# Performance work log

Measured on AMD Instinct MI355X. Metric: run time of the kernel, lower is better.

Reference implementation:

```python
import jax, jax.numpy as jnp
import numpy as np

BETA = 1e-7

def pearson_corr(x, y):
    # torch.std is Bessel-corrected (ddof=1); corr clamped to [-1,1]
    n = x.shape[-1]
    cx = x - jnp.mean(x, axis=-1, keepdims=True)
    cy = y - jnp.mean(y, axis=-1, keepdims=True)
    cov = jnp.sum(cx * cy, axis=-1, keepdims=True) / (n - 1)
    xs = jnp.std(x, axis=-1, keepdims=True, ddof=1)
    ys = jnp.std(y, axis=-1, keepdims=True, ddof=1)
    return jnp.clip(cov / (xs * ys + BETA), -1.0, 1.0)

def pearson_loss(p, t):
    return jnp.mean(1.0 - pearson_corr(p, t))

def self_cos_sim(x):
    # x: [B,T,C] -> cosine-similarity map [B,T,T]
    num = jnp.einsum('btc,bsc->bts', x, x)
    d = jnp.sqrt(jnp.sum(x * x, axis=-1, keepdims=True))  # [B,T,1]
    den = d @ jnp.swapaxes(d, 1, 2)                        # [B,T,T]
    return num / den

def turn_into_waves(ssm):
    # Assumed Turn_map_into_waves: average SSM rows -> [B,T]
    return jnp.mean(ssm, axis=1)

def psd(x):
    # Assumed FFT_Batch: power spectrum along last dim
    return jnp.abs(jnp.fft.rfft(x, axis=-1)) ** 2

def loss_distill_pyramid(on_ssm, tg_ssm):
    w_on = turn_into_waves(on_ssm)
    w_tg = turn_into_waves(tg_ssm)
    mse = jnp.mean((on_ssm - tg_ssm) ** 2) + jnp.mean((w_on - w_tg) ** 2)
    return mse + pearson_loss(on_ssm, tg_ssm) + pearson_loss(w_on, w_tg)

def loss_reg(ssm):
    # Vectorized replacement of per-diagonal nested loops + torch.std.
    # For offset k in [1, n-2]: std over the k-th superdiagonal (m = n-k
    # elements, Bessel-corrected), scaled by m/20; mean over offsets & batch.
    n = ssm.shape[-1]
    ii, jj = np.triu_indices(n, k=1)
    seg = jj - ii - 1                               # segment = offset-1 in [0, n-2]
    onehot = jax.nn.one_hot(jnp.asarray(seg), n - 1, dtype=ssm.dtype)  # [M, n-1]
    vals = ssm[:, ii, jj]                           # [B, M] upper-tri gather
    s1 = vals @ onehot                              # per-diagonal sums   [B, n-1]
    s2 = (vals * vals) @ onehot                     # per-diagonal sum-sq [B, n-1]
    m = jnp.asarray(n - 1 - np.arange(n - 1), dtype=ssm.dtype)
    var = jnp.where(m > 1, (s2 - s1 * s1 / m) / jnp.maximum(m - 1, 1.0), 0.0)
    std = jnp.sqrt(jnp.maximum(var, 0.0)) * m / 20.0
    return jnp.mean(std[:, : n - 2])                # original drops last diagonal

def loss_freq(ssm):
    waves = turn_into_waves(ssm)
    p = psd(waves)
    L = p.shape[-1]
    lf, hf = int(0.5 * L / 30.0), int(3 * L / 30.0)
    p = p[:, : L // 2]
    p = p / jnp.max(p, axis=-1, keepdims=True)
    return jnp.mean(jnp.sum(p, axis=-1) / jnp.sum(p[:, lf:hf], axis=-1) - 1.0)

def loss_distill_rppg(on, tg):
    temporal = pearson_loss(on, tg)
    L = on.shape[-1]
    lf, hf, vhf = int(0.5 * L / 30.0), int(3 * L / 30.0), int(15 * L / 30.0)
    so = psd(on)[:, :vhf]
    st = psd(tg)[:, :vhf]
    so = so / jnp.max(so, axis=-1, keepdims=True)
    st = st / jnp.max(st, axis=-1, keepdims=True)
    partition = jnp.sum(so, axis=-1) / jnp.sum(so[:, lf:hf], axis=-1) - 1.0
    return temporal + pearson_loss(so, st) + jnp.mean(partition)

def setup_inputs() -> dict:
    key = jax.random.key(0)
    k1, k2, k3, k4 = jax.random.split(key, 4)
    B, T, C, L = 128, 256, 768, 576
    return {
        'pyr_online': jax.random.normal(k1, (B, T, C), dtype=jnp.float32),
        'pyr_target': jax.random.normal(k2, (B, T, C), dtype=jnp.float32),
        'rppg_online': jax.random.normal(k3, (B, L), dtype=jnp.float32),
        'rppg_target': jax.random.normal(k4, (B, L), dtype=jnp.float32),
    }

def reference(pyr_online, pyr_target, rppg_online, rppg_target):
    tg_ssm = self_cos_sim(jax.lax.stop_gradient(pyr_target))
    on_ssm = self_cos_sim(pyr_online)
    loss_pyramid = loss_distill_pyramid(on_ssm, tg_ssm) * 0.5
    loss_r = loss_reg(on_ssm) * 0.5          # single pyramid level (len=1)
    loss_f = loss_freq(on_ssm) * 0.2
    loss_rppg = loss_distill_rppg(rppg_online, jax.lax.stop_gradient(rppg_target)) * 0.5
    total = loss_rppg + loss_pyramid + loss_r + loss_f
    return (total, loss_pyramid, loss_rppg, loss_r, loss_f)
```

## Files before the change

### kernel.cpp

```cpp
#include <hip/hip_runtime.h>
#include <hip/hip_bf16.h>

#define NB 128
#define NT 256
#define NC 768
#define NL 576

constexpr size_t OFF_P1    = 4096;
constexpr size_t OFF_WON   = 135168;
constexpr size_t OFF_WTG   = 167936;
constexpr size_t OFF_PW    = 200704;
constexpr size_t OFF_FRQ   = 200960;
constexpr size_t OFF_FREQR = 209152;
constexpr size_t OFF_RG    = 209280;
constexpr size_t OFF_RPG   = 241920;
constexpr size_t OFF_SO    = 242304;
constexpr size_t OFF_ST    = 279168;
constexpr size_t OFF_SSM_ON_B = (size_t)2 * 1024 * 1024;
constexpr size_t OFF_SSM_TG_B = OFF_SSM_ON_B + (size_t)NB * NT * NT * 2;

typedef __attribute__((ext_vector_type(8))) short short8v;
typedef __attribute__((ext_vector_type(4))) float f32x4;

__device__ __forceinline__ unsigned short f2bf(float f) {
    __hip_bfloat16 h = __float2bfloat16(f);
    unsigned short u; __builtin_memcpy(&u, &h, 2); return u;
}
__device__ __forceinline__ float bf2f(unsigned short u) {
    __hip_bfloat16 h; __builtin_memcpy(&h, &u, 2); return __bfloat162float(h);
}

__device__ __forceinline__ float sin2pi(float x) {
    x -= floorf(x + 0.5f);
    float x2 = x * x;
    float p = 3.8199526f;
    p = p * x2 - 15.094643f;
    p = p * x2 + 42.058693f;
    p = p * x2 - 76.705860f;
    p = p * x2 + 81.605249f;
    p = p * x2 - 41.341702f;
    p = p * x2 + 6.2831853f;
    return p * x;
}
__device__ __forceinline__ float cos2pi(float x) { return sin2pi(x + 0.25f); }

__device__ __forceinline__ float blockSum(float v, float* tmp) {
    int lane = threadIdx.x & 63, wid = threadIdx.x >> 6;
#pragma unroll
    for (int o = 32; o; o >>= 1) v += __shfl_down(v, o, 64);
    __syncthreads();
    if (lane == 0) tmp[wid] = v;
    __syncthreads();
    return tmp[0] + tmp[1] + tmp[2] + tmp[3];
}
__device__ __forceinline__ float blockMax(float v, float* tmp) {
    int lane = threadIdx.x & 63, wid = threadIdx.x >> 6;
#pragma unroll
    for (int o = 32; o; o >>= 1) v = fmaxf(v, __shfl_down(v, o, 64));
    __syncthreads();
    if (lane == 0) tmp[wid] = v;
    __syncthreads();
    return fmaxf(fmaxf(tmp[0], tmp[1]), fmaxf(tmp[2], tmp[3]));
}
__device__ __forceinline__ float pearson1m(float S0, float S1, float S2, float S3,
                                           float S4, float n) {
    float cov = (S4 - S0 * S1 / n) / (n - 1.f);
    float xs = sqrtf(fmaxf((S2 - S0 * S0 / n) / (n - 1.f), 0.f));
    float ys = sqrtf(fmaxf((S3 - S1 * S1 / n) / (n - 1.f), 0.f));
    float corr = fminf(1.f, fmaxf(-1.f, cov / (xs * ys + 1e-7f)));
    return 1.f - corr;
}

__device__ __forceinline__ float stage32(unsigned short* dstrow, const float* p, int sw) {
    float sq = 0.f;
#pragma unroll
    for (int half = 0; half < 2; half++) {
        float4 a = *reinterpret_cast<const float4*>(p + 16 * half);
        float4 b = *reinterpret_cast<const float4*>(p + 16 * half + 4);
        float4 c = *reinterpret_cast<const float4*>(p + 16 * half + 8);
        float4 d = *reinterpret_cast<const float4*>(p + 16 * half + 12);
        sq += a.x * a.x + a.y * a.y + a.z * a.z + a.w * a.w;
        sq += b.x * b.x + b.y * b.y + b.z * b.z + b.w * b.w;
        sq += c.x * c.x + c.y * c.y + c.z * c.z + c.w * c.w;
        sq += d.x * d.x + d.y * d.y + d.z * d.z + d.w * d.w;
        short8v v0, v1;
        v0[0] = (short)f2bf(a.x); v0[1] = (short)f2bf(a.y);
        v0[2] = (short)f2bf(a.z); v0[3] = (short)f2bf(a.w);
        v0[4] = (short)f2bf(b.x); v0[5] = (short)f2bf(b.y);
        v0[6] = (short)f2bf(b.z); v0[7] = (short)f2bf(b.w);
        v1[0] = (short)f2bf(c.x); v1[1] = (short)f2bf(c.y);
        v1[2] = (short)f2bf(c.z); v1[3] = (short)f2bf(c.w);
        v1[4] = (short)f2bf(d.x); v1[5] = (short)f2bf(d.y);
        v1[6] = (short)f2bf(d.z); v1[7] = (short)f2bf(d.w);
        *reinterpret_cast<short8v*>(dstrow + 8 * ((2 * half) ^ sw)) = v0;
        *reinterpret_cast<short8v*>(dstrow + 8 * ((2 * half + 1) ^ sw)) = v1;
    }
    return sq;
}

__global__ __launch_bounds__(256, 4) void gram3_k(const float* __restrict__ on,
                                                  const float* __restrict__ tg,
                                                  unsigned short* __restrict__ ssm_on,
                                                  unsigned short* __restrict__ ssm_tg) {
    __shared__ unsigned short lds[2][256][32];
    __shared__ float invs[256];
    int lin = blockIdx.x;
    int x = lin & 7, g = lin >> 3;
    int pair = x * 32 + (g >> 2);
    int tile = g & 3;
    int b = pair >> 1, tau = pair & 1;
    int rt = tile >> 1, ct = tile & 1;
    const float* X = tau ? tg : on;
    unsigned short* S = (tau ? ssm_tg : ssm_on) + (size_t)b * NT * NT;

    int t = threadIdx.x;
    int wave = t >> 6, lane = t & 63;
    int fr = lane & 15, fq = lane >> 4;
    int wr = (wave >> 1) * 64, wc = (wave & 1) * 64;

    const float* src = X + ((size_t)b * NT + t) * NC;
    int sw = (t >> 1) & 3;
    float sq = 0.f;

    int arow = rt * 128 + wr + fr;
    int brow = ct * 128 + wc + fr;
    int aswz = fq ^ ((fr >> 1) & 3);
    int acol = 8 * aswz;

    f32x4 acc[4][4] = {};

    sq += stage32(&lds[0][t][0], src, sw);
    __syncthreads();
    int cur = 0;
#pragma unroll 1
    for (int s = 0; s < 24; s++) {
        short8v A0 = *reinterpret_cast<short8v*>(&lds[cur][arow][acol]);
        short8v A1 = *reinterpret_cast<short8v*>(&lds[cur][arow + 16][acol]);
        short8v A2 = *reinterpret_cast<short8v*>(&lds[cur][arow + 32][acol]);
        short8v A3 = *reinterpret_cast<short8v*>(&lds[cur][arow + 48][acol]);
        short8v B0 = *reinterpret_cast<short8v*>(&lds[cur][brow][acol]);
        short8v B1 = *reinterpret_cast<short8v*>(&lds[cur][brow + 16][acol]);
        short8v B2 = *reinterpret_cast<short8v*>(&lds[cur][brow + 32][acol]);
        short8v B3 = *reinterpret_cast<short8v*>(&lds[cur][brow + 48][acol]);
        acc[0][0] = __builtin_amdgcn_mfma_f32_16x16x32_bf16(A0, B0, acc[0][0], 0, 0, 0);
        acc[0][1] = __builtin_amdgcn_mfma_f32_16x16x32_bf16(A0, B1, acc[0][1], 0, 0, 0);
        acc[0][2] = __builtin_amdgcn_mfma_f32_16x16x32_bf16(A0, B2, acc[0][2], 0, 0, 0);
        acc[0][3] = __builtin_amdgcn_mfma_f32_16x16x32_bf16(A0, B3, acc[0][3], 0, 0, 0);
        acc[1][0] = __builtin_amdgcn_mfma_f32_16x16x32_bf16(A1, B0, acc[1][0], 0, 0, 0);
        acc[1][1] = __builtin_amdgcn_mfma_f32_16x16x32_bf16(A1, B1, acc[1][1], 0, 0, 0);
        acc[1][2] = __builtin_amdgcn_mfma_f32_16x16x32_bf16(A1, B2, acc[1][2], 0, 0, 0);
        acc[1][3] = __builtin_amdgcn_mfma_f32_16x16x32_bf16(A1, B3, acc[1][3], 0, 0, 0);
        acc[2][0] = __builtin_amdgcn_mfma_f32_16x16x32_bf16(A2, B0, acc[2][0], 0, 0, 0);
        acc[2][1] = __builtin_amdgcn_mfma_f32_16x16x32_bf16(A2, B1, acc[2][1], 0, 0, 0);
        acc[2][2] = __builtin_amdgcn_mfma_f32_16x16x32_bf16(A2, B2, acc[2][2], 0, 0, 0);
        acc[2][3] = __builtin_amdgcn_mfma_f32_16x16x32_bf16(A2, B3, acc[2][3], 0, 0, 0);
        acc[3][0] = __builtin_amdgcn_mfma_f32_16x16x32_bf16(A3, B0, acc[3][0], 0, 0, 0);
        acc[3][1] = __builtin_amdgcn_mfma_f32_16x16x32_bf16(A3, B1, acc[3][1], 0, 0, 0);
        acc[3][2] = __builtin_amdgcn_mfma_f32_16x16x32_bf16(A3, B2, acc[3][2], 0, 0, 0);
        acc[3][3] = __builtin_amdgcn_mfma_f32_16x16x32_bf16(A3, B3, acc[3][3], 0, 0, 0);
        if (s < 23) sq += stage32(&lds[cur ^ 1][t][0], src + 32 * (s + 1), sw);
        __syncthreads();
        cur ^= 1;
    }
    invs[t] = 1.f / sqrtf(sq);
    __syncthreads();
#pragma unroll
    for (int f = 0; f < 4; f++) {
        int row0 = rt * 128 + wr + 16 * f + 4 * fq;
#pragma unroll
        for (int gg = 0; gg < 4; gg++) {
            int col = ct * 128 + wc + 16 * gg + fr;
            float ic = invs[col];
#pragma unroll
            for (int r = 0; r < 4; r++)
                S[(size_t)(row0 + r) * NT + col] = f2bf(acc[f][gg][r] * invs[row0 + r] * ic);
        }
    }
}

__global__ __launch_bounds__(256) void pearson256w_k(const unsigned short* __restrict__ A,
                                                     const unsigned short* __restrict__ Bv,
                                                     float* __restrict__ part,
                                                     float* __restrict__ won,
                                                     float* __restrict__ wtg) {
    size_t base = (size_t)blockIdx.x * NT;
    int tid = threadIdx.x;
    float o = bf2f(A[base + tid]), g = bf2f(Bv[base + tid]);
    __shared__ float tmp[4];
    float S0 = blockSum(o, tmp);
    float S1 = blockSum(g, tmp);
    float S2 = blockSum(o * o, tmp);
    float S3 = blockSum(g * g, tmp);
    float S4 = blockSum(o * g, tmp);
    float S5 = blockSum((o - g) * (o - g), tmp);
    if (tid == 0) {
        part[2 * blockIdx.x + 0] = pearson1m(S0, S1, S2, S3, S4, 256.f);
        part[2 * blockIdx.x + 1] = S5;
        won[blockIdx.x] = S0 * (1.f / NT);
        wtg[blockIdx.x] = S1 * (1.f / NT);
    }
}

__global__ __launch_bounds__(256) void pearsonW_k(const float* __restrict__ A,
                                                  const float* __restrict__ Bv,
                                                  float* __restrict__ part) {
    size_t base = (size_t)blockIdx.x * NT;
    int tid = threadIdx.x;
    float o = A[base + tid], g = Bv[base + tid];
    __shared__ float tmp[4];
    float S0 = blockSum(o, tmp);
    float S1 = blockSum(g, tmp);
    float S2 = blockSum(o * o, tmp);
    float S3 = blockSum(g * g, tmp);
    float S4 = blockSum(o * g, tmp);
    float S5 = blockSum((o - g) * (o - g), tmp);
    if (tid == 0) {
        part[2 * blockIdx.x + 0] = pearson1m(S0, S1, S2, S3, S4, 256.f);
        part[2 * blockIdx.x + 1] = S5;
    }
}

__global__ __launch_bounds__(256) void freqbin_k(const float* __restrict__ w,
                                                 float* __restrict__ frq) {
    int k = blockIdx.x, b = blockIdx.y, m = threadIdx.x;
    float val = w[b * NT + m];
    float x = (float)((m * k) & 255) * (1.f / 256.f);
    __shared__ float tmp[4];
    float re = blockSum(val * cos2pi(x), tmp);
    float im = blockSum(val * sin2pi(x), tmp);
    if (m == 0) frq[b * 64 + k] = re * re + im * im;
}

__global__ __launch_bounds__(256) void freqfin_k(const float* __restrict__ frq,
                                                 float* __restrict__ fr) {
    int b = blockIdx.x, t = threadIdx.x;
    float v = (t < 64) ? frq[b * 64 + t] : 0.f;
    float vb = (t >= 2 && t < 12) ? v : 0.f;
    __shared__ float tmp[4];
    float Ft = blockSum(v, tmp);
    float Fb = blockSum(vb, tmp);
    if (t == 0) fr[b] = (Fb > 0.f) ? (Ft / Fb - 1.f) : 0.f;
}

__global__ __launch_bounds__(256) void regdiag_k(const unsigned short* __restrict__ ssm,
                                                 float* __restrict__ rg) {
    int d = blockIdx.x + 1, b = blockIdx.y, i = threadIdx.x;
    int col = i + d;
    bool ok = col < 256;
    float v = 0.f;
    if (ok) v = bf2f(ssm[(size_t)b * NT * NT + i * NT + col]);
    __shared__ float tmp[4];
    float s1 = blockSum(v, tmp);
    float s2 = blockSum(v * v, tmp);
    if (i == 0) {
        float outv = 0.f;
        if (d <= 254) {
            float m = (float)(256 - d);
            float var = (s2 - s1 * s1 / m) / (m - 1.f);
            outv = sqrtf(fmaxf(var, 0.f)) * m * 0.05f;
        }
        rg[b * 255 + (d - 1)] = outv;
    }
}

__global__ __launch_bounds__(256) void rppgT_k(const float* __restrict__ on,
                                               const float* __restrict__ tg,
                                               float* __restrict__ tq) {
    int b = blockIdx.x, t = threadIdx.x;
    const float* po = on + (size_t)b * NL;
    const float* pg = tg + (size_t)b * NL;
    float o1 = po[t], g1 = pg[t], o2 = po[t + 256], g2 = pg[t + 256];
    bool h3 = t < 64;
    float o3 = h3 ? po[t + 512] : 0.f, g3 = h3 ? pg[t + 512] : 0.f;
    __shared__ float tmp[4];
    float S0 = blockSum(o1 + o2 + o3, tmp);
    float S1 = blockSum(g1 + g2 + g3, tmp);
    float S2 = blockSum(o1 * o1 + o2 * o2 + o3 * o3, tmp);
    float S3 = blockSum(g1 * g1 + g2 * g2 + g3 * g3, tmp);
    float S4 = blockSum(o1 * g1 + o2 * g2 + o3 * g3, tmp);
    if (t == 0) tq[3 * b + 0] = pearson1m(S0, S1, S2, S3, S4, 576.f);
}

__global__ __launch_bounds__(256) void rppgbin_k(const float* __restrict__ on,
                                                 const float* __restrict__ tg,
                                                 float* __restrict__ so,
                                                 float* __restrict__ st) {
    int k = blockIdx.x, b = blockIdx.y, t = threadIdx.x;
    float reo = 0.f, imo = 0.f, reg_ = 0.f, img = 0.f;
#pragma unroll
    for (int p = 0; p < 3; p++) {
        int m = t + 256 * p;
        if (m < NL) {
            float x = (float)((m * k) % NL) * (1.f / 576.f);
            float c = cos2pi(x), s = sin2pi(x);
            float o = on[(size_t)b * NL + m], g = tg[(size_t)b * NL + m];
            reo = fmaf(o, c, reo); imo = fmaf(o, s, imo);
            reg_ = fmaf(g, c, reg_); img = fmaf(g, s, img);
        }
    }
    __shared__ float tmp[4];
    float RO = blockSum(reo, tmp);
    float IO = blockSum(imo, tmp);
    float RG = blockSum(reg_, tmp);
    float IG = blockSum(img, tmp);
    if (t == 0) {
        so[b * 288 + k] = RO * RO + IO * IO;
        st[b * 288 + k] = RG * RG + IG * IG;
    }
}

__global__ __launch_bounds__(256) void rppgfin_k(const float* __restrict__ so,
                                                 const float* __restrict__ st,
                                                 float* __restrict__ tq) {
    int b = blockIdx.x, t = threadIdx.x;
    const float* SO = so + (size_t)b * 288;
    const float* ST = st + (size_t)b * 288;
    float a0 = SO[t], b0 = ST[t];
    bool h2 = t < 32;
    float a1 = h2 ? SO[t + 256] : 0.f, b1 = h2 ? ST[t + 256] : 0.f;
    __shared__ float tmp[4];
    float Mo = blockMax(fmaxf(a0, a1), tmp);
    float Mg = blockMax(fmaxf(b0, b1), tmp);
    if (Mo <= 0.f) Mo = 1.f;
    if (Mg <= 0.f) Mg = 1.f;
    float n0 = a0 / Mo, m0 = b0 / Mg;
    float n1 = a1 / Mo, m1 = b1 / Mg;
    float S0 = blockSum(n0 + n1, tmp);
    float S1 = blockSum(m0 + m1, tmp);
    float S2 = blockSum(n0 * n0 + n1 * n1, tmp);
    float S3 = blockSum(m0 * m0 + m1 * m1, tmp);
    float S4 = blockSum(n0 * m0 + n1 * m1, tmp);
    float bt0 = (t >= 9 && t < 57) ? a0 : 0.f;
    float TT = blockSum(a0 + a1, tmp);
    float TB = blockSum(bt0, tmp);
    if (t == 0) {
        tq[3 * b + 1] = pearson1m(S0, S1, S2, S3, S4, 288.f);
        tq[3 * b + 2] = (TB > 0.f) ? (TT / TB - 1.f) : 0.f;
    }
}

__global__ __launch_bounds__(256) void final_k(const float* __restrict__ ws,
                                               float* __restrict__ out) {
    __shared__ float tmp[4];
    int tid = threadIdx.x;
    const float* p1 = ws + OFF_P1;
    float a = 0.f, bsum = 0.f;
    for (int i = tid; i < 32768; i += 256) { a += p1[2 * i]; bsum += p1[2 * i + 1]; }
    float S0 = blockSum(a, tmp);
    float S1 = blockSum(bsum, tmp);
    const float* pw = ws + OFF_PW;
    float c0 = 0.f, c1 = 0.f;
    for (int i = tid; i < 128; i += 256) { c0 += pw[2 * i]; c1 += pw[2 * i + 1]; }
    float W0 = blockSum(c0, tmp);
    float W1 = blockSum(c1, tmp);
    const float* fr = ws + OFF_FREQR;
    float f = (tid < 128) ? fr[tid] : 0.f;
    float Fq = blockSum(f, tmp);
    const float* rg = ws + OFF_RG;
    float e = 0.f;
    for (int i = tid; i < 32640; i += 256) e += rg[i];
    float Rg = blockSum(e, tmp);
    const float* tq = ws + OFF_RPG;
    float g0 = 0.f, g1 = 0.f, g2 = 0.f;
    for (int i = tid; i < 128; i += 256) {
        g0 += tq[3 * i]; g1 += tq[3 * i + 1]; g2 += tq[3 * i + 2];
    }
    float R0 = blockSum(g0, tmp);
    float R1 = blockSum(g1, tmp);
    float R2 = blockSum(g2, tmp);
    if (tid == 0) {
        float loss_pyr  = 0.5f * (S1 / 8388608.f + W1 / 32768.f + S0 / 32768.f + W0 / 128.f);
        float loss_r    = 0.5f * Rg / (128.f * 254.f);
        float loss_f    = 0.2f * Fq / 128.f;
        float loss_rppg = 0.5f * (R0 + R1 + R2) / 128.f;
        float total = loss_rppg + loss_pyr + loss_r + loss_f;
        out[0] = total;
        out[1] = loss_pyr;
        out[2] = loss_rppg;
        out[3] = loss_r;
        out[4] = loss_f;
    }
}

extern "C" void kernel_launch(void* const* d_in, const int* in_sizes, int n_in,
                              void* d_out, int out_size, void* d_ws, size_t ws_size,
                              hipStream_t stream) {
    const float* pyr_on  = (const float*)d_in[0];
    const float* pyr_tg  = (const float*)d_in[1];
    const float* rppg_on = (const float*)d_in[2];
    const float* rppg_tg = (const float*)d_in[3];
    float* ws = (float*)d_ws;
    unsigned short* ssm_on = (unsigned short*)((char*)d_ws + OFF_SSM_ON_B);
    unsigned short* ssm_tg = (unsigned short*)((char*)d_ws + OFF_SSM_TG_B);
    float* out = (float*)d_out;

    gram3_k<<<1024, 256, 0, stream>>>(pyr_on, pyr_tg, ssm_on, ssm_tg);
    pearson256w_k<<<32768, 256, 0, stream>>>(ssm_on, ssm_tg, ws + OFF_P1,
                                             ws + OFF_WON, ws + OFF_WTG);
    pearsonW_k<<<NB, 256, 0, stream>>>(ws + OFF_WON, ws + OFF_WTG, ws + OFF_PW);
    freqbin_k<<<dim3(64, NB), 256, 0, stream>>>(ws + OFF_WON, ws + OFF_FRQ);
    freqfin_k<<<NB, 256, 0, stream>>>(ws + OFF_FRQ, ws + OFF_FREQR);
    regdiag_k<<<dim3(255, NB), 256, 0, stream>>>(ssm_on, ws + OFF_RG);
    rppgT_k<<<NB, 256, 0, stream>>>(rppg_on, rppg_tg, ws + OFF_RPG);
    rppgbin_k<<<dim3(288, NB), 256, 0, stream>>>(rppg_on, rppg_tg, ws + OFF_SO, ws + OFF_ST);
    rppgfin_k<<<NB, 256, 0, stream>>>(ws + OFF_SO, ws + OFF_ST, ws + OFF_RPG);
    final_k<<<1, 256, 0, stream>>>(ws, out);
}
```

Measured before the change: 318.7 us.

## Shrink gram tiles to 64x64 with register prefetch; per-batch diagonal-std kernel

The Gram/cosine kernel now uses 64x64 output tiles across 4096 blocks instead of 128x128 across 1024. Each block loads only its row and column strips, with global loads prefetched into registers ahead of the MFMAs, and row norms reduced through shuffles. This gives more blocks and occupancy at the cost of re-reading the input more often and recomputing norms. The diagonal-std regularizer drops from 255x128 blocks to one block per batch that accumulates per-diagonal sums with LDS atomics. That reduces launch size and the final reduction but serialises 255 row iterations inside each block.

```diff
diff --git a/kernel.cpp b/kernel.cpp
--- a/kernel.cpp
+++ b/kernel.cpp
@@ -12,7 +12,7 @@
 constexpr size_t OFF_PW    = 200704;
 constexpr size_t OFF_FRQ   = 200960;
 constexpr size_t OFF_FREQR = 209152;
-constexpr size_t OFF_RG    = 209280;
+constexpr size_t OFF_REGB  = 209280;
 constexpr size_t OFF_RPG   = 241920;
 constexpr size_t OFF_SO    = 242304;
 constexpr size_t OFF_ST    = 279168;
@@ -20,6 +20,7 @@
 constexpr size_t OFF_SSM_TG_B = OFF_SSM_ON_B + (size_t)NB * NT * NT * 2;
 
 typedef __attribute__((ext_vector_type(8))) short short8v;
+typedef __attribute__((ext_vector_type(4))) short short4v;
 typedef __attribute__((ext_vector_type(4))) float f32x4;
 
 __device__ __forceinline__ unsigned short f2bf(float f) {
@@ -71,109 +72,111 @@
     return 1.f - corr;
 }
 
-__device__ __forceinline__ float stage32(unsigned short* dstrow, const float* p, int sw) {
-    float sq = 0.f;
-#pragma unroll
-    for (int half = 0; half < 2; half++) {
-        float4 a = *reinterpret_cast<const float4*>(p + 16 * half);
-        float4 b = *reinterpret_cast<const float4*>(p + 16 * half + 4);
-        float4 c = *reinterpret_cast<const float4*>(p + 16 * half + 8);
-        float4 d = *reinterpret_cast<const float4*>(p + 16 * half + 12);
-        sq += a.x * a.x + a.y * a.y + a.z * a.z + a.w * a.w;
-        sq += b.x * b.x + b.y * b.y + b.z * b.z + b.w * b.w;
-        sq += c.x * c.x + c.y * c.y + c.z * c.z + c.w * c.w;
-        sq += d.x * d.x + d.y * d.y + d.z * d.z + d.w * d.w;
-        short8v v0, v1;
-        v0[0] = (short)f2bf(a.x); v0[1] = (short)f2bf(a.y);
-        v0[2] = (short)f2bf(a.z); v0[3] = (short)f2bf(a.w);
-        v0[4] = (short)f2bf(b.x); v0[5] = (short)f2bf(b.y);
-        v0[6] = (short)f2bf(b.z); v0[7] = (short)f2bf(b.w);
-        v1[0] = (short)f2bf(c.x); v1[1] = (short)f2bf(c.y);
-        v1[2] = (short)f2bf(c.z); v1[3] = (short)f2bf(c.w);
-        v1[4] = (short)f2bf(d.x); v1[5] = (short)f2bf(d.y);
-        v1[6] = (short)f2bf(d.z); v1[7] = (short)f2bf(d.w);
-        *reinterpret_cast<short8v*>(dstrow + 8 * ((2 * half) ^ sw)) = v0;
-        *reinterpret_cast<short8v*>(dstrow + 8 * ((2 * half + 1) ^ sw)) = v1;
-    }
-    return sq;
-}
-
-__global__ __launch_bounds__(256, 4) void gram3_k(const float* __restrict__ on,
+#define LDS_HALF (128 * 32)
+__global__ __launch_bounds__(256, 6) void gram5_k(const float* __restrict__ on,
                                                   const float* __restrict__ tg,
                                                   unsigned short* __restrict__ ssm_on,
                                                   unsigned short* __restrict__ ssm_tg) {
-    __shared__ unsigned short lds[2][256][32];
-    __shared__ float invs[256];
+    __shared__ unsigned short lds[2 * LDS_HALF];
+    __shared__ float invs[128];
     int lin = blockIdx.x;
-    int x = lin & 7, g = lin >> 3;
-    int pair = x * 32 + (g >> 2);
-    int tile = g & 3;
+    int xcd = lin & 7, m = lin >> 3;
+    int pair = (m >> 4) * 8 + xcd;
+    int tile = m & 15;
+    int rt = tile >> 2, ct = tile & 3;
     int b = pair >> 1, tau = pair & 1;
-    int rt = tile >> 1, ct = tile & 1;
     const float* X = tau ? tg : on;
     unsigned short* S = (tau ? ssm_tg : ssm_on) + (size_t)b * NT * NT;
 
     int t = threadIdx.x;
     int wave = t >> 6, lane = t & 63;
     int fr = lane & 15, fq = lane >> 4;
-    int wr = (wave >> 1) * 64, wc = (wave & 1) * 64;
-
-    const float* src = X + ((size_t)b * NT + t) * NC;
-    int sw = (t >> 1) & 3;
-    float sq = 0.f;
-
-    int arow = rt * 128 + wr + fr;
-    int brow = ct * 128 + wc + fr;
-    int aswz = fq ^ ((fr >> 1) & 3);
-    int acol = 8 * aswz;
-
-    f32x4 acc[4][4] = {};
-
-    sq += stage32(&lds[0][t][0], src, sw);
-    __syncthreads();
+    int wr = (wave >> 1) * 32, wc = (wave & 1) * 32;
+
+    int c = t & 7;
+    const float* rowp[4];
+    int ldsoff[4];
+    float sq[4] = {0.f, 0.f, 0.f, 0.f};
+#pragma unroll
+    for (int p = 0; p < 4; p++) {
+        int lr = (t >> 3) + 32 * p;
+        int grow = (lr < 64) ? (rt * 64 + lr) : (ct * 64 + (lr - 64));
+        rowp[p] = X + ((size_t)b * NT + grow) * NC + 4 * c;
+        ldsoff[p] = lr * 32 + (((c >> 1) ^ ((lr >> 1) & 3)) << 3) + ((c & 1) << 2);
+    }
+    int aswz = (fq ^ ((fr >> 1) & 3)) << 3;
+    int offA0 = (wr + fr) * 32 + aswz;
+    int offA1 = (wr + 16 + fr) * 32 + aswz;
+    int offB0 = (64 + wc + fr) * 32 + aswz;
+    int offB1 = (64 + wc + 16 + fr) * 32 + aswz;
+
+    f32x4 acc[2][2] = {};
+
+#pragma unroll
+    for (int p = 0; p < 4; p++) {
+        float4 u = *reinterpret_cast<const float4*>(rowp[p]);
+        sq[p] += u.x * u.x + u.y * u.y + u.z * u.z + u.w * u.w;
+        short4v v;
+        v[0] = (short)f2bf(u.x); v[1] = (short)f2bf(u.y);
+        v[2] = (short)f2bf(u.z); v[3] = (short)f2bf(u.w);
+        *reinterpret_cast<short4v*>(&lds[ldsoff[p]]) = v;
+    }
+    __syncthreads();
+
     int cur = 0;
 #pragma unroll 1
     for (int s = 0; s < 24; s++) {
-        short8v A0 = *reinterpret_cast<short8v*>(&lds[cur][arow][acol]);
-        short8v A1 = *reinterpret_cast<short8v*>(&lds[cur][arow + 16][acol]);
-        short8v A2 = *reinterpret_cast<short8v*>(&lds[cur][arow + 32][acol]);
-        short8v A3 = *reinterpret_cast<short8v*>(&lds[cur][arow + 48][acol]);
-        short8v B0 = *reinterpret_cast<short8v*>(&lds[cur][brow][acol]);
-        short8v B1 = *reinterpret_cast<short8v*>(&lds[cur][brow + 16][acol]);
-        short8v B2 = *reinterpret_cast<short8v*>(&lds[cur][brow + 32][acol]);
-        short8v B3 = *reinterpret_cast<short8v*>(&lds[cur][brow + 48][acol]);
+        unsigned short* rb = &lds[cur * LDS_HALF];
+        short8v A0 = *reinterpret_cast<short8v*>(rb + offA0);
+        short8v A1 = *reinterpret_cast<short8v*>(rb + offA1);
+        short8v B0 = *reinterpret_cast<short8v*>(rb + offB0);
+        short8v B1 = *reinterpret_cast<short8v*>(rb + offB1);
+        float4 u[4];
+        if (s < 23) {
+#pragma unroll
+            for (int p = 0; p < 4; p++)
+                u[p] = *reinterpret_cast<const float4*>(rowp[p] + 32 * (s + 1));
+        }
         acc[0][0] = __builtin_amdgcn_mfma_f32_16x16x32_bf16(A0, B0, acc[0][0], 0, 0, 0);
         acc[0][1] = __builtin_amdgcn_mfma_f32_16x16x32_bf16(A0, B1, acc[0][1], 0, 0, 0);
-        acc[0][2] = __builtin_amdgcn_mfma_f32_16x16x32_bf16(A0, B2, acc[0][2], 0, 0, 0);
-        acc[0][3] = __builtin_amdgcn_mfma_f32_16x16x32_bf16(A0, B3, acc[0][3], 0, 0, 0);
         acc[1][0] = __builtin_amdgcn_mfma_f32_16x16x32_bf16(A1, B0, acc[1][0], 0, 0, 0);
         acc[1][1] = __builtin_amdgcn_mfma_f32_16x16x32_bf16(A1, B1, acc[1][1], 0, 0, 0);
-        acc[1][2] = __builtin_amdgcn_mfma_f32_16x16x32_bf16(A1, B2, acc[1][2], 0, 0, 0);
-        acc[1][3] = __builtin_amdgcn_mfma_f32_16x16x32_bf16(A1, B3, acc[1][3], 0, 0, 0);
-        acc[2][0] = __builtin_amdgcn_mfma_f32_16x16x32_bf16(A2, B0, acc[2][0], 0, 0, 0);
-        acc[2][1] = __builtin_amdgcn_mfma_f32_16x16x32_bf16(A2, B1, acc[2][1], 0, 0, 0);
-        acc[2][2] = __builtin_amdgcn_mfma_f32_16x16x32_bf16(A2, B2, acc[2][2], 0, 0, 0);
-        acc[2][3] = __builtin_amdgcn_mfma_f32_16x16x32_bf16(A2, B3, acc[2][3], 0, 0, 0);
-        acc[3][0] = __builtin_amdgcn_mfma_f32_16x16x32_bf16(A3, B0, acc[3][0], 0, 0, 0);
-        acc[3][1] = __builtin_amdgcn_mfma_f32_16x16x32_bf16(A3, B1, acc[3][1], 0, 0, 0);
-        acc[3][2] = __builtin_amdgcn_mfma_f32_16x16x32_bf16(A3, B2, acc[3][2], 0, 0, 0);
-        acc[3][3] = __builtin_amdgcn_mfma_f32_16x16x32_bf16(A3, B3, acc[3][3], 0, 0, 0);
-        if (s < 23) sq += stage32(&lds[cur ^ 1][t][0], src + 32 * (s + 1), sw);
+        if (s < 23) {
+            unsigned short* wbuf = &lds[(cur ^ 1) * LDS_HALF];
+#pragma unroll
+            for (int p = 0; p < 4; p++) {
+                sq[p] += u[p].x * u[p].x + u[p].y * u[p].y +
+                         u[p].z * u[p].z + u[p].w * u[p].w;
+                short4v v;
+                v[0] = (short)f2bf(u[p].x); v[1] = (short)f2bf(u[p].y);
+                v[2] = (short)f2bf(u[p].z); v[3] = (short)f2bf(u[p].w);
+                *reinterpret_cast<short4v*>(wbuf + ldsoff[p]) = v;
+            }
+        }
         __syncthreads();
         cur ^= 1;
     }
-    invs[t] = 1.f / sqrtf(sq);
-    __syncthreads();
-#pragma unroll
-    for (int f = 0; f < 4; f++) {
-        int row0 = rt * 128 + wr + 16 * f + 4 * fq;
-#pragma unroll
-        for (int gg = 0; gg < 4; gg++) {
-            int col = ct * 128 + wc + 16 * gg + fr;
-            float ic = invs[col];
+#pragma unroll
+    for (int p = 0; p < 4; p++) {
+        float v = sq[p];
+        v += __shfl_down(v, 4, 8);
+        v += __shfl_down(v, 2, 8);
+        v += __shfl_down(v, 1, 8);
+        if (c == 0) invs[(t >> 3) + 32 * p] = 1.f / sqrtf(v);
+    }
+    __syncthreads();
+#pragma unroll
+    for (int f = 0; f < 2; f++) {
+        int rowl = wr + 16 * f + 4 * fq;
+#pragma unroll
+        for (int g = 0; g < 2; g++) {
+            int coll = wc + 16 * g + fr;
+            float ic = invs[64 + coll];
+            int gcol = ct * 64 + coll;
 #pragma unroll
             for (int r = 0; r < 4; r++)
-                S[(size_t)(row0 + r) * NT + col] = f2bf(acc[f][gg][r] * invs[row0 + r] * ic);
+                S[(size_t)(rt * 64 + rowl + r) * NT + gcol] =
+                    f2bf(acc[f][g][r] * invs[rowl + r] * ic);
         }
     }
 }
@@ -242,25 +245,31 @@
     if (t == 0) fr[b] = (Fb > 0.f) ? (Ft / Fb - 1.f) : 0.f;
 }
 
-__global__ __launch_bounds__(256) void regdiag_k(const unsigned short* __restrict__ ssm,
-                                                 float* __restrict__ rg) {
-    int d = blockIdx.x + 1, b = blockIdx.y, i = threadIdx.x;
-    int col = i + d;
-    bool ok = col < 256;
-    float v = 0.f;
-    if (ok) v = bf2f(ssm[(size_t)b * NT * NT + i * NT + col]);
-    __shared__ float tmp[4];
-    float s1 = blockSum(v, tmp);
-    float s2 = blockSum(v * v, tmp);
-    if (i == 0) {
-        float outv = 0.f;
-        if (d <= 254) {
-            float m = (float)(256 - d);
-            float var = (s2 - s1 * s1 / m) / (m - 1.f);
-            outv = sqrtf(fmaxf(var, 0.f)) * m * 0.05f;
+__global__ __launch_bounds__(256) void regbin_k(const unsigned short* __restrict__ ssm,
+                                                float* __restrict__ preg) {
+    __shared__ float s1[256], s2[256];
+    __shared__ float tmp[4];
+    int b = blockIdx.x, t = threadIdx.x;
+    const unsigned short* S = ssm + (size_t)b * NT * NT;
+    s1[t] = 0.f; s2[t] = 0.f;
+    __syncthreads();
+    for (int i = 0; i < 255; i++) {
+        float v = bf2f(S[i * NT + t]);
+        if (t > i) {
+            int d = t - i - 1;
+            atomicAdd(&s1[d], v);
+            atomicAdd(&s2[d], v * v);
         }
-        rg[b * 255 + (d - 1)] = outv;
-    }
+    }
+    __syncthreads();
+    float stdv = 0.f;
+    if (t < 254) {
+        float mm = (float)(255 - t);
+        float var = (s2[t] - s1[t] * s1[t] / mm) / (mm - 1.f);
+        stdv = sqrtf(fmaxf(var, 0.f)) * mm * 0.05f;
+    }
+    float R = blockSum(stdv, tmp);
+    if (t == 0) preg[b] = R;
 }
 
 __global__ __launch_bounds__(256) void rppgT_k(const float* __restrict__ on,
@@ -292,10 +301,10 @@
         int m = t + 256 * p;
         if (m < NL) {
             float x = (float)((m * k) % NL) * (1.f / 576.f);
-            float c = cos2pi(x), s = sin2pi(x);
+            float cc = cos2pi(x), ss = sin2pi(x);
             float o = on[(size_t)b * NL + m], g = tg[(size_t)b * NL + m];
-            reo = fmaf(o, c, reo); imo = fmaf(o, s, imo);
-            reg_ = fmaf(g, c, reg_); img = fmaf(g, s, img);
+            reo = fmaf(o, cc, reo); imo = fmaf(o, ss, imo);
+            reg_ = fmaf(g, cc, reg_); img = fmaf(g, ss, img);
         }
     }
     __shared__ float tmp[4];
@@ -356,9 +365,8 @@
     const float* fr = ws + OFF_FREQR;
     float f = (tid < 128) ? fr[tid] : 0.f;
     float Fq = blockSum(f, tmp);
-    const float* rg = ws + OFF_RG;
-    float e = 0.f;
-    for (int i = tid; i < 32640; i += 256) e += rg[i];
+    const float* rb = ws + OFF_REGB;
+    float e = (tid < 128) ? rb[tid] : 0.f;
     float Rg = blockSum(e, tmp);
     const float* tq = ws + OFF_RPG;
     float g0 = 0.f, g1 = 0.f, g2 = 0.f;
@@ -394,13 +402,13 @@
     unsigned short* ssm_tg = (unsigned short*)((char*)d_ws + OFF_SSM_TG_B);
     float* out = (float*)d_out;
 
-    gram3_k<<<1024, 256, 0, stream>>>(pyr_on, pyr_tg, ssm_on, ssm_tg);
+    gram5_k<<<4096, 256, 0, stream>>>(pyr_on, pyr_tg, ssm_on, ssm_tg);
     pearson256w_k<<<32768, 256, 0, stream>>>(ssm_on, ssm_tg, ws + OFF_P1,
                                              ws + OFF_WON, ws + OFF_WTG);
     pearsonW_k<<<NB, 256, 0, stream>>>(ws + OFF_WON, ws + OFF_WTG, ws + OFF_PW);
     freqbin_k<<<dim3(64, NB), 256, 0, stream>>>(ws + OFF_WON, ws + OFF_FRQ);
     freqfin_k<<<NB, 256, 0, stream>>>(ws + OFF_FRQ, ws + OFF_FREQR);
-    regdiag_k<<<dim3(255, NB), 256, 0, stream>>>(ssm_on, ws + OFF_RG);
+    regbin_k<<<NB, 256, 0, stream>>>(ssm_on, ws + OFF_REGB);
     rppgT_k<<<NB, 256, 0, stream>>>(rppg_on, rppg_tg, ws + OFF_RPG);
     rppgbin_k<<<dim3(288, NB), 256, 0, stream>>>(rppg_on, rppg_tg, ws + OFF_SO, ws + OFF_ST);
     rppgfin_k<<<NB, 256, 0, stream>>>(ws + OFF_SO, ws + OFF_ST, ws + OFF_RPG);
```

Result: slower. 347.2 us (+9.0%).
